# Performance work log

Measured on AMD Instinct MI355X. Metric: run time of the kernel, lower is better.

The kernel has to match this reference:

```python
import jax, jax.numpy as jnp
import numpy as np

N = 16384   # total queries (= total keys here)
B = 16      # scenes
K = 1024    # keys per scene (key_batch_cnt entries)
L = 32      # local neighborhood size
D = 256     # d_model
H = 8       # nhead
DFF = 1024
LN_EPS = 1e-5


def setup_inputs() -> dict:
    key = jax.random.key(0)
    ks = jax.random.split(key, 32)
    f32 = jnp.float32

    def lin(k, o, i):
        return jax.random.normal(k, (o, i), f32) * 0.02

    idx = jax.random.randint(ks[3], (N, L), 0, K)
    invalid = jax.random.uniform(ks[4], (N, L)) < 0.1
    index_pair = jnp.where(invalid, -1, idx).astype(jnp.int32)

    inp = {
        "tgt": jax.random.normal(ks[0], (N, D), f32),
        "memory": jax.random.normal(ks[1], (N, D), f32),
        "memory_pos_emb": jax.random.normal(ks[2], (N, D), f32),
        "key_batch_cnt": jnp.full((B,), K, dtype=jnp.int32),
        "index_pair": index_pair,
        "index_pair_batch": jnp.repeat(jnp.arange(B, dtype=jnp.int32), K),
        "Wq": lin(ks[5], D, D), "bq": jnp.zeros((D,), f32),
        "Wkc": lin(ks[6], D, D), "bkc": jnp.zeros((D,), f32),
        "Wkp": lin(ks[7], D, D), "bkp": jnp.zeros((D,), f32),
        "Wv": lin(ks[8], D, D), "bv": jnp.zeros((D,), f32),
        "Wo": lin(ks[9], D, D), "bo": jnp.zeros((D,), f32),
        "W1": lin(ks[10], DFF, D), "b1": jnp.zeros((DFF,), f32),
        "W2": lin(ks[11], D, DFF), "b2": jnp.zeros((D,), f32),
        "g2": jnp.ones((D,), f32), "be2": jnp.zeros((D,), f32),
        "g3": jnp.ones((D,), f32), "be3": jnp.zeros((D,), f32),
    }
    return inp


def _ln(x, g, b):
    m = jnp.mean(x, axis=-1, keepdims=True)
    v = jnp.mean((x - m) ** 2, axis=-1, keepdims=True)
    return (x - m) * jax.lax.rsqrt(v + LN_EPS) * g + b


def reference(tgt, memory, memory_pos_emb, key_batch_cnt, index_pair,
              index_pair_batch, Wq, bq, Wkc, bkc, Wkp, bkp, Wv, bv,
              Wo, bo, W1, b1, W2, b2, g2, be2, g3, be3):
    Dh = D // H
    scale = Dh ** -0.5

    # dense projections
    q = tgt @ Wq.T + bq                              # [N, D]
    k = (memory @ Wkc.T + bkc) + (memory_pos_emb @ Wkp.T + bkp)  # content + pos
    v = memory @ Wv.T + bv

    # local-index gather: per-batch indices -> global key indices
    offsets = jnp.concatenate([jnp.zeros((1,), jnp.int32),
                               jnp.cumsum(key_batch_cnt)[:-1].astype(jnp.int32)])
    mask = index_pair < 0                            # [N, L] padded neighbors
    gidx = jnp.where(mask, 0, index_pair + offsets[index_pair_batch][:, None])

    kg = k[gidx].reshape(N, L, H, Dh)                # gathered keys  [N,L,H,Dh]
    vg = v[gidx].reshape(N, L, H, Dh)                # gathered values
    qh = q.reshape(N, H, Dh)

    attn = jnp.einsum('nhd,nlhd->nhl', qh, kg) * scale
    attn = jnp.where(mask[:, None, :], -1e9, attn)
    attn = jax.nn.softmax(attn, axis=-1)
    out = jnp.einsum('nhl,nlhd->nhd', attn, vg).reshape(N, D)
    tgt2 = out @ Wo.T + bo                           # attention out_proj

    x = _ln(tgt + tgt2, g2, be2)
    ff = jax.nn.relu(x @ W1.T + b1) @ W2.T + b2
    return _ln(x + ff, g3, be3)
```

## Files before the change

### kernel.cpp

```cpp
#include <hip/hip_runtime.h>
#include <stdint.h>

#define N_TOT 16384
#define LNEI  32
#define DM    256
#define NH    8
#define DH    32
#define DFF   1024

typedef __attribute__((ext_vector_type(8))) short  short8;
typedef __attribute__((ext_vector_type(4))) float  floatx4;
typedef __attribute__((ext_vector_type(2))) float  float2_t;
typedef __attribute__((ext_vector_type(4))) int    intx4;
typedef __attribute__((ext_vector_type(4))) unsigned short ushort4_t;
typedef __attribute__((ext_vector_type(4))) unsigned int uint4_t;

#if defined(__has_builtin)
#if __has_builtin(__builtin_amdgcn_fdot2_f32_bf16)
#define HAS_DOT2 1
#endif
#endif
#ifndef HAS_DOT2
#define HAS_DOT2 0
#endif

#if HAS_DOT2
typedef __attribute__((ext_vector_type(2))) __bf16 bf16x2_t;
#endif

static __device__ __forceinline__ float b2f(unsigned short u) {
  union { unsigned int u; float f; } x; x.u = ((unsigned int)u) << 16; return x.f;
}
static __device__ __forceinline__ unsigned short f2b(float f) {
  union { float f; unsigned int u; } x; x.f = f;
  unsigned int r = x.u + 0x7fffu + ((x.u >> 16) & 1u);
  return (unsigned short)(r >> 16);
}
static __device__ __forceinline__ float lo16(unsigned int d) {
  union { unsigned int u; float f; } x; x.u = d << 16; return x.f;
}
static __device__ __forceinline__ float hi16(unsigned int d) {
  union { unsigned int u; float f; } x; x.u = d & 0xffff0000u; return x.f;
}

#define NSEG 11
struct Seg { const float* src; unsigned short* dst; int cols; int ostride; int ooff; int begin; };
struct SegTable { Seg s[NSEG]; int total; };

__global__ __launch_bounds__(256) void cvt_all(SegTable T, float* biaskv,
                                               const float* bkc, const float* bkp,
                                               const float* bv) {
  int e = (blockIdx.x * 256 + threadIdx.x) * 4;
  if (e >= T.total) {
    int c = e - T.total;
    #pragma unroll
    for (int j = 0; j < 4; ++j, ++c)
      if (c < 512) biaskv[c] = (c < 256) ? (bkc[c] + bkp[c]) : bv[c - 256];
    return;
  }
  int si = 0;
  #pragma unroll
  for (int i = 1; i < NSEG; ++i) if (e >= T.s[i].begin) si = i;
  const Seg s = T.s[si];
  const int le = e - s.begin;
  const int row = le / s.cols;
  const int col = le - row * s.cols;
  floatx4 v = {0.f, 0.f, 0.f, 0.f};
  if (s.src) v = *(const floatx4*)(s.src + le);
  ushort4_t o;
  o.x = f2b(v[0]); o.y = f2b(v[1]); o.z = f2b(v[2]); o.w = f2b(v[3]);
  *(ushort4_t*)(s.dst + (size_t)row * s.ostride + s.ooff + col) = o;
}

static __device__ __forceinline__ void gl_lds16(const unsigned short* g, unsigned short* l) {
  __builtin_amdgcn_global_load_lds(
      (const __attribute__((address_space(1))) unsigned int*)g,
      (__attribute__((address_space(3))) unsigned int*)l, 16, 0, 0);
}

template<int BN, bool RELU>
static __device__ __forceinline__ void gemm_body(
    const unsigned short* __restrict__ A, const unsigned short* __restrict__ W,
    const float* __restrict__ bias, unsigned short* __restrict__ C,
    int Nd, int K, int lda, int m0, int n0,
    unsigned short* sA, unsigned short* sB)
{
  constexpr int BM = 128, BK = 32;
  constexpr int MI = (BN == 128) ? 4 : 2;
  constexpr int NI = 4;
  constexpr int sAh = BM * BK, sBh = BN * BK;

  const int w    = threadIdx.x >> 6;
  const int lane = threadIdx.x & 63;
  const int quad = lane >> 4;
  const int l16  = lane & 15;
  const int wrow0 = (BN == 128) ? (w >> 1) * 64 : w * 32;
  const int wcol0 = (BN == 128) ? (w & 1) * 64 : 0;

  const int aflat0 = w * 512 + lane * 8;
  const int ar0 = aflat0 >> 5, ac = aflat0 & 31;

  floatx4 acc[MI][NI] = {};

  for (int k0 = 0; k0 < K; k0 += 2 * BK) {
    __syncthreads();
    #pragma unroll
    for (int half = 0; half < 2; ++half) {
      const int kk = k0 + half * BK;
      #pragma unroll
      for (int c = 0; c < 2; ++c) {
        const int row = ar0 + c * 64;
        gl_lds16(A + (size_t)(m0 + row) * lda + kk + ac, sA + half * sAh + (c * 4 + w) * 512);
      }
      if (BN == 128) {
        #pragma unroll
        for (int c = 0; c < 2; ++c) {
          const int row = ar0 + c * 64;
          gl_lds16(W + (size_t)(n0 + row) * K + kk + ac, sB + half * sBh + (c * 4 + w) * 512);
        }
      } else {
        gl_lds16(W + (size_t)(n0 + ar0) * K + kk + ac, sB + half * sBh + w * 512);
      }
    }
    __syncthreads();

    #pragma unroll
    for (int half = 0; half < 2; ++half) {
      short8 af[MI], bf[NI];
      #pragma unroll
      for (int mi = 0; mi < MI; ++mi)
        af[mi] = *(const short8*)&sA[half * sAh + (wrow0 + mi * 16 + l16) * BK + quad * 8];
      #pragma unroll
      for (int ni = 0; ni < NI; ++ni)
        bf[ni] = *(const short8*)&sB[half * sBh + (wcol0 + ni * 16 + l16) * BK + quad * 8];
      #pragma unroll
      for (int mi = 0; mi < MI; ++mi)
        #pragma unroll
        for (int ni = 0; ni < NI; ++ni)
          acc[mi][ni] = __builtin_amdgcn_mfma_f32_16x16x32_bf16(af[mi], bf[ni], acc[mi][ni], 0, 0, 0);
    }
  }

  #pragma unroll
  for (int ni = 0; ni < NI; ++ni) {
    const int col = n0 + wcol0 + ni * 16 + l16;
    const float bvv = bias[col];
    #pragma unroll
    for (int mi = 0; mi < MI; ++mi) {
      const int row0 = m0 + wrow0 + mi * 16 + quad * 4;
      #pragma unroll
      for (int i = 0; i < 4; ++i) {
        float v = acc[mi][ni][i] + bvv;
        if (RELU) v = fmaxf(v, 0.f);
        C[(size_t)(row0 + i) * Nd + col] = f2b(v);
      }
    }
  }
}

template<int BN, bool RELU>
__global__ __launch_bounds__(256) void gemm_tile(
    const unsigned short* __restrict__ A, const unsigned short* __restrict__ W,
    const float* __restrict__ bias,
    unsigned short* __restrict__ C, int M, int Nd, int K, int lda)
{
  __shared__ unsigned short sA[2 * 128 * 32];
  __shared__ unsigned short sB[2 * BN * 32];
  gemm_body<BN, RELU>(A, W, bias, C, Nd, K, lda,
                      blockIdx.x * 128, blockIdx.y * BN, sA, sB);
}

__global__ __launch_bounds__(256) void gemm_qkv(
    const unsigned short* __restrict__ tgt_b, const unsigned short* __restrict__ Wq_b,
    const float* __restrict__ bq, unsigned short* __restrict__ q_b,
    const unsigned short* __restrict__ mp_b, const unsigned short* __restrict__ Wkv_b,
    const float* __restrict__ bias_kv, unsigned short* __restrict__ kv_b)
{
  __shared__ unsigned short sA[2 * 128 * 32];
  __shared__ unsigned short sB[2 * 64 * 32];
  const int m0 = blockIdx.x * 128;
  if (blockIdx.y < 4)
    gemm_body<64, false>(tgt_b, Wq_b, bq, q_b, 256, 256, 256,
                         m0, blockIdx.y * 64, sA, sB);
  else
    gemm_body<64, false>(mp_b, Wkv_b, bias_kv, kv_b, 512, 512, 512,
                         m0, (blockIdx.y - 4) * 64, sA, sB);
}

__global__ __launch_bounds__(256) void attn_kernel(
    const unsigned short* __restrict__ q, const unsigned short* __restrict__ kv,
    const int* __restrict__ key_batch_cnt, const int* __restrict__ index_pair,
    const int* __restrict__ index_pair_batch,
    unsigned short* __restrict__ out)
{
  const int n = ((blockIdx.x & 7) << 11) | (blockIdx.x >> 3);
  const int t = threadIdx.x;
  __shared__ unsigned short s_qb[DM];
#if !HAS_DOT2
  __shared__ float s_qf[DM];
#endif
  __shared__ int   s_gidx[LNEI];
  __shared__ int   s_goff[LNEI];
  __shared__ float s_score[NH][LNEI];
  __shared__ float s_prob[NH][LNEI];
  __shared__ float s_out[2][DM];

  const unsigned short qr = q[(size_t)n * DM + t];
  s_qb[t] = qr;
#if !HAS_DOT2
  s_qf[t] = b2f(qr);
#endif
  if (t < 64) {
    const int b = index_pair_batch[n];
    int cnt = (t < 16) ? key_batch_cnt[t] : 0;
    cnt = (t < b) ? cnt : 0;
    #pragma unroll
    for (int msk = 32; msk >= 1; msk >>= 1) cnt += __shfl_xor(cnt, msk, 64);
    if (t < LNEI) {
      const int ip = index_pair[(size_t)n * LNEI + t];
      const int gi = (ip < 0) ? -1 : (ip + cnt);
      s_gidx[t] = gi;
      s_goff[t] = (gi < 0 ? 0 : gi) << 10;
    }
  }
  __syncthreads();

  {
    const int j  = t >> 3;
    const int c8 = t & 7;
    const int g  = s_gidx[j];
    const char* kbase = (const char*)kv + s_goff[j];

    float part[4];
    #pragma unroll
    for (int i = 0; i < 4; ++i) {
      const int c = c8 + i * 8;
      const uint4_t d = *(const uint4_t*)(kbase + c * 16);
#if HAS_DOT2
      union { uint4_t u; bf16x2_t p[4]; } ku, qu;
      ku.u = d;
      qu.u = *(const uint4_t*)&s_qb[c * 8];
      float acc = 0.f;
      #pragma unroll
      for (int r = 0; r < 4; ++r)
        acc = __builtin_amdgcn_fdot2_f32_bf16(ku.p[r], qu.p[r], acc, false);
      part[i] = acc;
#else
      const float* qp = &s_qf[c * 8];
      part[i] = lo16(d.x) * qp[0] + hi16(d.x) * qp[1]
              + lo16(d.y) * qp[2] + hi16(d.y) * qp[3]
              + lo16(d.z) * qp[4] + hi16(d.z) * qp[5]
              + lo16(d.w) * qp[6] + hi16(d.w) * qp[7];
#endif
    }
    #pragma unroll
    for (int i = 0; i < 4; ++i) {
      part[i] += __shfl_xor(part[i], 1, 64);
      part[i] += __shfl_xor(part[i], 2, 64);
    }
    if ((c8 & 3) == 0) {
      const int hodd = c8 >> 2;
      #pragma unroll
      for (int i = 0; i < 4; ++i)
        s_score[2 * i + hodd][j] =
            (g < 0) ? -1e9f : part[i] * 0.17677669529663687f;
    }
  }
  __syncthreads();

  {
    const int h = t >> 5;
    const int l = t & 31;
    const float sc = s_score[h][l];
    float mx = sc;
    #pragma unroll
    for (int msk = 16; msk >= 1; msk >>= 1) mx = fmaxf(mx, __shfl_xor(mx, msk, 64));
    const float e = __expf(sc - mx);
    float sm = e;
    #pragma unroll
    for (int msk = 16; msk >= 1; msk >>= 1) sm += __shfl_xor(sm, msk, 64);
    s_prob[h][l] = e / sm;
  }
  __syncthreads();

  {
    const int jh  = t >> 7;
    const int h   = (t >> 4) & 7;
    const int dh2 = t & 15;
    floatx4 p4[4];
    intx4   o4[4];
    #pragma unroll
    for (int r = 0; r < 4; ++r) {
      p4[r] = *(const floatx4*)&s_prob[h][jh * 16 + r * 4];
      o4[r] = *(const intx4*)&s_goff[jh * 16 + r * 4];
    }
    float2_t acc = {0.f, 0.f};
    const char* vbase = (const char*)kv + 512 + h * 64 + dh2 * 4;
    #pragma unroll
    for (int j2 = 0; j2 < 16; ++j2) {
      const int off = o4[j2 >> 2][j2 & 3];
      const float p = p4[j2 >> 2][j2 & 3];
      const unsigned int d = *(const unsigned int*)(vbase + off);
      acc = __builtin_elementwise_fma((float2_t){p, p},
                                      (float2_t){lo16(d), hi16(d)}, acc);
    }
    s_out[jh][h * DH + dh2 * 2]     = acc[0];
    s_out[jh][h * DH + dh2 * 2 + 1] = acc[1];
  }
  __syncthreads();

  out[(size_t)n * DM + t] = f2b(s_out[0][t] + s_out[1][t]);
}

template<bool IN1F32, bool OUTF32>
__global__ __launch_bounds__(256) void ln_kernel(
    const void* __restrict__ in1, const unsigned short* __restrict__ in2,
    const float* __restrict__ g, const float* __restrict__ b,
    void* __restrict__ out)
{
  const int n    = blockIdx.x * 4 + (threadIdx.x >> 6);
  const int lane = threadIdx.x & 63;
  const int c0   = lane * 4;

  float a[4];
  if (IN1F32) {
    const floatx4 v = *(const floatx4*)((const float*)in1 + (size_t)n * DM + c0);
    a[0] = v[0]; a[1] = v[1]; a[2] = v[2]; a[3] = v[3];
  } else {
    const ushort4_t u = *(const ushort4_t*)((const unsigned short*)in1 + (size_t)n * DM + c0);
    a[0] = b2f(u.x); a[1] = b2f(u.y); a[2] = b2f(u.z); a[3] = b2f(u.w);
  }
  {
    const ushort4_t u = *(const ushort4_t*)(in2 + (size_t)n * DM + c0);
    a[0] += b2f(u.x); a[1] += b2f(u.y); a[2] += b2f(u.z); a[3] += b2f(u.w);
  }

  float s = a[0] + a[1] + a[2] + a[3];
  #pragma unroll
  for (int msk = 32; msk >= 1; msk >>= 1) s += __shfl_xor(s, msk, 64);
  const float mean = s * (1.0f / DM);

  float d[4], s2 = 0.f;
  #pragma unroll
  for (int i = 0; i < 4; ++i) { d[i] = a[i] - mean; s2 += d[i] * d[i]; }
  #pragma unroll
  for (int msk = 32; msk >= 1; msk >>= 1) s2 += __shfl_xor(s2, msk, 64);
  const float r = rsqrtf(s2 * (1.0f / DM) + 1e-5f);

  const floatx4 gv = *(const floatx4*)(g + c0);
  const floatx4 bv = *(const floatx4*)(b + c0);
  if (OUTF32) {
    floatx4 y;
    #pragma unroll
    for (int i = 0; i < 4; ++i) y[i] = d[i] * r * gv[i] + bv[i];
    *((floatx4*)((float*)out + (size_t)n * DM + c0)) = y;
  } else {
    ushort4_t y;
    y.x = f2b(d[0] * r * gv[0] + bv[0]);
    y.y = f2b(d[1] * r * gv[1] + bv[1]);
    y.z = f2b(d[2] * r * gv[2] + bv[2]);
    y.w = f2b(d[3] * r * gv[3] + bv[3]);
    *((ushort4_t*)((unsigned short*)out + (size_t)n * DM + c0)) = y;
  }
}

extern "C" void kernel_launch(void* const* d_in, const int* in_sizes, int n_in,
                              void* d_out, int out_size, void* d_ws, size_t ws_size,
                              hipStream_t stream) {
  const float* tgt  = (const float*)d_in[0];
  const float* mem  = (const float*)d_in[1];
  const float* pos  = (const float*)d_in[2];
  const int* kbc    = (const int*)d_in[3];
  const int* ipair  = (const int*)d_in[4];
  const int* ipb    = (const int*)d_in[5];
  const float* Wq   = (const float*)d_in[6];
  const float* bq   = (const float*)d_in[7];
  const float* Wkc  = (const float*)d_in[8];
  const float* bkc  = (const float*)d_in[9];
  const float* Wkp  = (const float*)d_in[10];
  const float* bkp  = (const float*)d_in[11];
  const float* Wv   = (const float*)d_in[12];
  const float* bvp  = (const float*)d_in[13];
  const float* Wo   = (const float*)d_in[14];
  const float* bo   = (const float*)d_in[15];
  const float* W1   = (const float*)d_in[16];
  const float* b1   = (const float*)d_in[17];
  const float* W2   = (const float*)d_in[18];
  const float* b2   = (const float*)d_in[19];
  const float* g2   = (const float*)d_in[20];
  const float* be2  = (const float*)d_in[21];
  const float* g3   = (const float*)d_in[22];
  const float* be3  = (const float*)d_in[23];

  const size_t NB = (size_t)N_TOT * DM;
  unsigned short* ws = (unsigned short*)d_ws;
  unsigned short* tgt_b = ws;
  unsigned short* ao_b  = ws;
  unsigned short* t2_b  = ws + NB;
  unsigned short* mp_b  = ws + 2 * NB;
  unsigned short* x_b   = ws + 2 * NB;
  unsigned short* ff_b  = ws + 3 * NB;
  unsigned short* q_b   = ws + 4 * NB;
  unsigned short* h1_b  = ws + 4 * NB;
  unsigned short* kv_b  = ws + 5 * NB;
  unsigned short* wgt   = ws + 8 * NB;
  unsigned short* Wq_b  = wgt;
  unsigned short* Wkv_b = wgt + 65536;
  unsigned short* Wo_b  = wgt + 65536 + 262144;
  unsigned short* W1_b  = wgt + 2 * 65536 + 262144;
  unsigned short* W2_b  = wgt + 2 * 65536 + 2 * 262144;
  float* bias_kv = (float*)(wgt + 2 * 65536 + 3 * 262144);

  SegTable T;
  int beg = 0, i = 0;
  auto seg = [&](const float* s, unsigned short* d, int cols, int ostride, int ooff, int nelem) {
    T.s[i].src = s; T.s[i].dst = d; T.s[i].cols = cols;
    T.s[i].ostride = ostride; T.s[i].ooff = ooff; T.s[i].begin = beg;
    beg += nelem; ++i;
  };
  seg(tgt, tgt_b, DM, DM, 0,   (int)NB);
  seg(mem, mp_b,  DM, 512, 0,  (int)NB);
  seg(pos, mp_b,  DM, 512, DM, (int)NB);
  seg(Wq,  Wq_b,  DM, DM, 0,   65536);
  seg(Wkc, Wkv_b, DM, 512, 0,  65536);
  seg(Wkp, Wkv_b, DM, 512, DM, 65536);
  seg(Wv,  Wkv_b + (size_t)256 * 512, DM, 512, 0, 65536);
  seg(nullptr, Wkv_b + (size_t)256 * 512, DM, 512, DM, 65536);
  seg(Wo,  Wo_b,  DM, DM, 0,   65536);
  seg(W1,  W1_b,  DM, DM, 0,   262144);
  seg(W2,  W2_b,  DFF, DFF, 0, 262144);
  T.total = beg;

  dim3 blk(256);
  cvt_all<<<dim3(T.total / 1024 + 1), blk, 0, stream>>>(T, bias_kv, bkc, bkp, bvp);

  dim3 gQKV(N_TOT / 128, 12);
  dim3 gQ(N_TOT / 128, DM / 64);
  dim3 gF(N_TOT / 128, DFF / 128);

  gemm_qkv<<<gQKV, blk, 0, stream>>>(tgt_b, Wq_b, bq, q_b, mp_b, Wkv_b, bias_kv, kv_b);
  attn_kernel<<<dim3(N_TOT), blk, 0, stream>>>(q_b, kv_b, kbc, ipair, ipb, ao_b);
  gemm_tile<64, false><<<gQ, blk, 0, stream>>>(ao_b, Wo_b, bo, t2_b, N_TOT, DM, DM, DM);
  ln_kernel<true, false><<<dim3(N_TOT / 4), blk, 0, stream>>>(tgt, t2_b, g2, be2, x_b);
  gemm_tile<128, true><<<gF, blk, 0, stream>>>(x_b, W1_b, b1, h1_b, N_TOT, DFF, DM, DM);
  gemm_tile<64, false><<<gQ, blk, 0, stream>>>(h1_b, W2_b, b2, ff_b, N_TOT, DM, DFF, DFF);
  ln_kernel<false, true><<<dim3(N_TOT / 4), blk, 0, stream>>>(x_b, ff_b, g3, be3, d_out);
}
```

Measured before the change: 252.7 us.

## Fuse output-projection and FFN2 GEMMs with residual add and LayerNorm

Adds a gemm_ln kernel where each block computes a full 64x256 output row tile with MFMA, then adds bias and residual and applies LayerNorm in registers using 16-lane shuffles. It replaces the Wo GEMM plus LN2 and the W2 GEMM plus LN3 pairs, removing two launches and the bf16 round trips of t2 and ff through global memory. In exchange the grid drops to 256 blocks with heavy register use (16 accumulators plus a 64-float x array), which can cut occupancy. The LN epilogue uses strided scalar stores, and variance is computed as E[x^2]-mean^2, which can lose precision.

Result: slower. 260.0 us (+2.9%).

```diff
diff --git a/kernel.cpp b/kernel.cpp
--- a/kernel.cpp
+++ b/kernel.cpp
@@ -187,6 +187,95 @@
                          m0, (blockIdx.y - 4) * 64, sA, sB);
 }
 
+template<bool RES_F32, bool OUT_F32>
+__global__ __launch_bounds__(256) void gemm_ln(
+    const unsigned short* __restrict__ A,
+    const unsigned short* __restrict__ W,
+    const float* __restrict__ bias,
+    const void* __restrict__ res,
+    const float* __restrict__ g, const float* __restrict__ be,
+    void* __restrict__ out,
+    int K)
+{
+  constexpr int BM = 64, Nd = 256, BK = 32;
+  constexpr int sAh = BM * BK, sBh = Nd * BK;
+  __shared__ unsigned short sA[2 * sAh];
+  __shared__ unsigned short sB[2 * sBh];
+
+  const int t    = threadIdx.x;
+  const int w    = t >> 6;
+  const int lane = t & 63;
+  const int quad = lane >> 4;
+  const int l16  = lane & 15;
+  const int m0   = blockIdx.x * BM;
+
+  const int aflat = t * 8;
+  const int ar = aflat >> 5, ac = aflat & 31;
+
+  floatx4 acc[16] = {};
+
+  for (int k0 = 0; k0 < K; k0 += 2 * BK) {
+    __syncthreads();
+    #pragma unroll
+    for (int half = 0; half < 2; ++half) {
+      const int kk = k0 + half * BK;
+      gl_lds16(A + (size_t)(m0 + ar) * K + kk + ac, &sA[half * sAh + aflat]);
+      #pragma unroll
+      for (int c = 0; c < 4; ++c) {
+        const int bflat = c * 2048 + t * 8;
+        const int br = bflat >> 5, bc = bflat & 31;
+        gl_lds16(W + (size_t)br * K + kk + bc, &sB[half * sBh + bflat]);
+      }
+    }
+    __syncthreads();
+    #pragma unroll
+    for (int half = 0; half < 2; ++half) {
+      const short8 af = *(const short8*)&sA[half * sAh + (w * 16 + l16) * BK + quad * 8];
+      #pragma unroll
+      for (int ni = 0; ni < 16; ++ni) {
+        const short8 bf = *(const short8*)&sB[half * sBh + (ni * 16 + l16) * BK + quad * 8];
+        acc[ni] = __builtin_amdgcn_mfma_f32_16x16x32_bf16(af, bf, acc[ni], 0, 0, 0);
+      }
+    }
+  }
+
+  const int row_base = m0 + w * 16 + quad * 4;
+  float x[4][16];
+  #pragma unroll
+  for (int ni = 0; ni < 16; ++ni) {
+    const int col = ni * 16 + l16;
+    const float bv = bias[col];
+    #pragma unroll
+    for (int i = 0; i < 4; ++i) {
+      float r;
+      if (RES_F32) r = ((const float*)res)[(size_t)(row_base + i) * Nd + col];
+      else         r = b2f(((const unsigned short*)res)[(size_t)(row_base + i) * Nd + col]);
+      x[i][ni] = acc[ni][i] + bv + r;
+    }
+  }
+  #pragma unroll
+  for (int i = 0; i < 4; ++i) {
+    float s = 0.f, s2 = 0.f;
+    #pragma unroll
+    for (int ni = 0; ni < 16; ++ni) { s += x[i][ni]; s2 += x[i][ni] * x[i][ni]; }
+    #pragma unroll
+    for (int msk = 8; msk >= 1; msk >>= 1) {
+      s  += __shfl_xor(s, msk, 64);
+      s2 += __shfl_xor(s2, msk, 64);
+    }
+    const float mean = s * (1.f / 256.f);
+    const float var  = s2 * (1.f / 256.f) - mean * mean;
+    const float rs   = rsqrtf(var + 1e-5f);
+    #pragma unroll
+    for (int ni = 0; ni < 16; ++ni) {
+      const int col = ni * 16 + l16;
+      const float y = (x[i][ni] - mean) * rs * g[col] + be[col];
+      if (OUT_F32) ((float*)out)[(size_t)(row_base + i) * Nd + col] = y;
+      else ((unsigned short*)out)[(size_t)(row_base + i) * Nd + col] = f2b(y);
+    }
+  }
+}
+
 __global__ __launch_bounds__(256) void attn_kernel(
     const unsigned short* __restrict__ q, const unsigned short* __restrict__ kv,
     const int* __restrict__ key_batch_cnt, const int* __restrict__ index_pair,
@@ -310,58 +399,6 @@
   __syncthreads();
 
   out[(size_t)n * DM + t] = f2b(s_out[0][t] + s_out[1][t]);
-}
-
-template<bool IN1F32, bool OUTF32>
-__global__ __launch_bounds__(256) void ln_kernel(
-    const void* __restrict__ in1, const unsigned short* __restrict__ in2,
-    const float* __restrict__ g, const float* __restrict__ b,
-    void* __restrict__ out)
-{
-  const int n    = blockIdx.x * 4 + (threadIdx.x >> 6);
-  const int lane = threadIdx.x & 63;
-  const int c0   = lane * 4;
-
-  float a[4];
-  if (IN1F32) {
-    const floatx4 v = *(const floatx4*)((const float*)in1 + (size_t)n * DM + c0);
-    a[0] = v[0]; a[1] = v[1]; a[2] = v[2]; a[3] = v[3];
-  } else {
-    const ushort4_t u = *(const ushort4_t*)((const unsigned short*)in1 + (size_t)n * DM + c0);
-    a[0] = b2f(u.x); a[1] = b2f(u.y); a[2] = b2f(u.z); a[3] = b2f(u.w);
-  }
-  {
-    const ushort4_t u = *(const ushort4_t*)(in2 + (size_t)n * DM + c0);
-    a[0] += b2f(u.x); a[1] += b2f(u.y); a[2] += b2f(u.z); a[3] += b2f(u.w);
-  }
-
-  float s = a[0] + a[1] + a[2] + a[3];
-  #pragma unroll
-  for (int msk = 32; msk >= 1; msk >>= 1) s += __shfl_xor(s, msk, 64);
-  const float mean = s * (1.0f / DM);
-
-  float d[4], s2 = 0.f;
-  #pragma unroll
-  for (int i = 0; i < 4; ++i) { d[i] = a[i] - mean; s2 += d[i] * d[i]; }
-  #pragma unroll
-  for (int msk = 32; msk >= 1; msk >>= 1) s2 += __shfl_xor(s2, msk, 64);
-  const float r = rsqrtf(s2 * (1.0f / DM) + 1e-5f);
-
-  const floatx4 gv = *(const floatx4*)(g + c0);
-  const floatx4 bv = *(const floatx4*)(b + c0);
-  if (OUTF32) {
-    floatx4 y;
-    #pragma unroll
-    for (int i = 0; i < 4; ++i) y[i] = d[i] * r * gv[i] + bv[i];
-    *((floatx4*)((float*)out + (size_t)n * DM + c0)) = y;
-  } else {
-    ushort4_t y;
-    y.x = f2b(d[0] * r * gv[0] + bv[0]);
-    y.y = f2b(d[1] * r * gv[1] + bv[1]);
-    y.z = f2b(d[2] * r * gv[2] + bv[2]);
-    y.w = f2b(d[3] * r * gv[3] + bv[3]);
-    *((ushort4_t*)((unsigned short*)out + (size_t)n * DM + c0)) = y;
-  }
 }
 
 extern "C" void kernel_launch(void* const* d_in, const int* in_sizes, int n_in,
@@ -396,10 +433,8 @@
   unsigned short* ws = (unsigned short*)d_ws;
   unsigned short* tgt_b = ws;
   unsigned short* ao_b  = ws;
-  unsigned short* t2_b  = ws + NB;
   unsigned short* mp_b  = ws + 2 * NB;
   unsigned short* x_b   = ws + 2 * NB;
-  unsigned short* ff_b  = ws + 3 * NB;
   unsigned short* q_b   = ws + 4 * NB;
   unsigned short* h1_b  = ws + 4 * NB;
   unsigned short* kv_b  = ws + 5 * NB;
@@ -435,14 +470,12 @@
   cvt_all<<<dim3(T.total / 1024 + 1), blk, 0, stream>>>(T, bias_kv, bkc, bkp, bvp);
 
   dim3 gQKV(N_TOT / 128, 12);
-  dim3 gQ(N_TOT / 128, DM / 64);
   dim3 gF(N_TOT / 128, DFF / 128);
+  dim3 gLN(N_TOT / 64);
 
   gemm_qkv<<<gQKV, blk, 0, stream>>>(tgt_b, Wq_b, bq, q_b, mp_b, Wkv_b, bias_kv, kv_b);
   attn_kernel<<<dim3(N_TOT), blk, 0, stream>>>(q_b, kv_b, kbc, ipair, ipb, ao_b);
-  gemm_tile<64, false><<<gQ, blk, 0, stream>>>(ao_b, Wo_b, bo, t2_b, N_TOT, DM, DM, DM);
-  ln_kernel<true, false><<<dim3(N_TOT / 4), blk, 0, stream>>>(tgt, t2_b, g2, be2, x_b);
+  gemm_ln<true, false><<<gLN, blk, 0, stream>>>(ao_b, Wo_b, bo, tgt, g2, be2, x_b, DM);
   gemm_tile<128, true><<<gF, blk, 0, stream>>>(x_b, W1_b, b1, h1_b, N_TOT, DFF, DM, DM);
-  gemm_tile<64, false><<<gQ, blk, 0, stream>>>(h1_b, W2_b, b2, ff_b, N_TOT, DM, DFF, DFF);
-  ln_kernel<false, true><<<dim3(N_TOT / 4), blk, 0, stream>>>(x_b, ff_b, g3, be3, d_out);
-}
+  gemm_ln<false, true><<<gLN, blk, 0, stream>>>(h1_b, W2_b, b2, x_b, g3, be3, d_out, DFF);
+}
```
